# Performance work log

Hardware: AMD Instinct MI355X
Metric: run time of the kernel (lower is better)

The kernel has to match this reference:

```python
import jax, jax.numpy as jnp
import numpy as np

B, H, W, DIM, HEADS, WS, SHIFT = 16, 64, 64, 512, 16, 8, 4
HEAD_DIM = DIM // HEADS
MLP_HID = 4 * DIM
N_WIN = (H // WS) * (W // WS)
NW = WS * WS  # tokens per window
SCALE = HEAD_DIM ** -0.5
LN_EPS = 1e-5


def _np_win_partition(x, ws):
    # replicates rearrange 'b (s1 h2) (s2 w2) c -> (b h2 w2) (s1 s2) c' (interleaved partition)
    b, h, w, c = x.shape
    h2, w2 = h // ws, w // ws
    x = x.reshape(b, ws, h2, ws, w2, c).transpose(0, 2, 4, 1, 3, 5)
    return x.reshape(b * h2 * w2, ws * ws, c)


def _build_mask():
    img = np.zeros((1, H, W, 1), np.float32)
    sl = [slice(0, -WS), slice(-WS, -SHIFT), slice(-SHIFT, None)]
    cnt = 0
    for hs in sl:
        for ws_ in sl:
            img[:, hs, ws_, :] = cnt
            cnt += 1
    wm = _np_win_partition(img, WS).reshape(-1, NW)  # (N_WIN, NW)
    diff = wm[:, None, :] - wm[:, :, None]
    mask = np.where(diff == 0, 1.0, 0.0).astype(np.float32)
    return (1.0 - mask) * -1e10  # (N_WIN, NW, NW) additive mask


def _rel_index():
    ch = np.arange(WS)
    coords = np.stack(np.meshgrid(ch, ch, indexing='ij')).reshape(2, -1)  # (2, NW)
    rel = (coords[:, :, None] - coords[:, None, :]).transpose(1, 2, 0)  # (NW, NW, 2)
    rel[..., 0] += WS - 1
    rel[..., 1] += WS - 1
    rel[..., 0] *= 2 * WS - 1
    return rel.sum(-1)  # (NW, NW) int


MASK = jnp.asarray(_build_mask())
REL_IDX = jnp.asarray(_rel_index().reshape(-1))


def _win_partition(x):  # (B, H, W, C) -> (B*N_WIN, NW, C)
    h2, w2 = H // WS, W // WS
    x = x.reshape(B, WS, h2, WS, w2, DIM).transpose(0, 2, 4, 1, 3, 5)
    return x.reshape(B * h2 * w2, WS * WS, DIM)


def _win_reverse(w):  # (B*N_WIN, NW, C) -> (B, H*W, C), inverse of the interleaved partition
    h2, w2 = H // WS, W // WS
    x = w.reshape(B, h2, w2, WS, WS, DIM).transpose(0, 3, 1, 4, 2, 5)
    return x.reshape(B, H * W, DIM)


def _ln(x, w, b):
    m = x.mean(-1, keepdims=True)
    v = jnp.mean((x - m) ** 2, axis=-1, keepdims=True)
    return (x - m) / jnp.sqrt(v + LN_EPS) * w + b


def setup_inputs() -> dict:
    key = jax.random.key(0)
    ks = jax.random.split(key, 6)
    std = 0.02
    return {
        'x': jax.random.normal(ks[0], (B, H * W, DIM), jnp.float32),
        'ln1_w': jnp.ones((DIM,), jnp.float32),
        'ln1_b': jnp.zeros((DIM,), jnp.float32),
        'qkv_w': jax.random.normal(ks[1], (3 * DIM, DIM), jnp.float32) * std,
        'qkv_b': jnp.zeros((3 * DIM,), jnp.float32),
        'rpb_table': jax.random.normal(ks[2], ((2 * WS - 1) ** 2, HEADS), jnp.float32) * std,
        'proj_w': jax.random.normal(ks[3], (DIM, DIM), jnp.float32) * std,
        'proj_b': jnp.zeros((DIM,), jnp.float32),
        'ln2_w': jnp.ones((DIM,), jnp.float32),
        'ln2_b': jnp.zeros((DIM,), jnp.float32),
        'fc1_w': jax.random.normal(ks[4], (MLP_HID, DIM), jnp.float32) * std,
        'fc1_b': jnp.zeros((MLP_HID,), jnp.float32),
        'fc2_w': jax.random.normal(ks[5], (DIM, MLP_HID), jnp.float32) * std,
        'fc2_b': jnp.zeros((DIM,), jnp.float32),
    }


def reference(x, ln1_w, ln1_b, qkv_w, qkv_b, rpb_table, proj_w, proj_b,
              ln2_w, ln2_b, fc1_w, fc1_b, fc2_w, fc2_b):
    h = x
    y = _ln(x, ln1_w, ln1_b).reshape(B, H, W, DIM)
    y = jnp.roll(y, (-SHIFT, -SHIFT), axis=(1, 2))  # cyclic shift
    xw = _win_partition(y)  # (B*N_WIN, NW, DIM)

    qkv = xw @ qkv_w.T + qkv_b  # (B*N_WIN, NW, 3*DIM)
    # original splits channel as (heads, head_dim, qkv) with qkv innermost
    qkv = qkv.reshape(B * N_WIN, NW, HEADS, HEAD_DIM, 3)
    q = qkv[..., 0].transpose(0, 2, 1, 3) * SCALE  # (Bw, H, NW, d)
    k = qkv[..., 1].transpose(0, 2, 1, 3)
    v = qkv[..., 2].transpose(0, 2, 1, 3)

    attn = jnp.einsum('bhqd,bhkd->bhqk', q, k)
    bias = rpb_table[REL_IDX].reshape(NW, NW, HEADS).transpose(2, 0, 1)  # (H, NW, NW)
    attn = attn + bias[None]
    # shift mask: per-window additive mask broadcast over batch and heads
    attn = attn.reshape(B, N_WIN, HEADS, NW, NW) + MASK[None, :, None]
    attn = jax.nn.softmax(attn, axis=-1).reshape(B * N_WIN, HEADS, NW, NW)

    out = jnp.einsum('bhqk,bhkd->bhqd', attn, v)
    out = out.transpose(0, 2, 1, 3).reshape(B * N_WIN, NW, DIM)
    out = out @ proj_w.T + proj_b

    attn_out = _win_reverse(out)  # (B, H*W, DIM)
    # NOTE: faithful to original - attention output is NOT rolled back before residual
    x2 = h + attn_out

    z = _ln(x2, ln2_w, ln2_b)
    z = jax.nn.gelu(z @ fc1_w.T + fc1_b, approximate=False)
    z = z @ fc2_w.T + fc2_b
    return x2 + z
```

## Files before the change

kernel.cpp:

```cpp
#include <hip/hip_runtime.h>
#include <math.h>

typedef short short8 __attribute__((ext_vector_type(8)));
typedef float f32x4 __attribute__((ext_vector_type(4)));
typedef unsigned short u16;
typedef u16 us4 __attribute__((ext_vector_type(4)));

#define DEVI static __device__ __forceinline__

constexpr float SCALE_Q = 0.17677669529663687f;

DEVI u16 f2bf(float f) {
  unsigned u = __builtin_bit_cast(unsigned, f);
  u += 0x7FFFu + ((u >> 16) & 1u);
  return (u16)(u >> 16);
}

DEVI void gload16(const u16* g, u16* l) {
  __builtin_amdgcn_global_load_lds((const __attribute__((address_space(1))) void*)g,
                                   (__attribute__((address_space(3))) void*)l,
                                   16, 0, 0);
}

__global__ void cvt_bf16(const float4* __restrict__ src, us4* __restrict__ dst, int n4) {
  int i = blockIdx.x * 256 + threadIdx.x;
  if (i < n4) {
    float4 v = src[i];
    us4 o = { f2bf(v.x), f2bf(v.y), f2bf(v.z), f2bf(v.w) };
    dst[i] = o;
  }
}

__global__ void cvt_qkvw(const float4* __restrict__ src, us4* __restrict__ dst) {
  int i = blockIdx.x * 256 + threadIdx.x;
  int row = i >> 7, c4 = i & 127;
  int which = row >> 9, head = (row >> 5) & 15, d = row & 31;
  int srow = head * 96 + d * 3 + which;
  float4 v = src[srow * 128 + c4];
  us4 o = { f2bf(v.x), f2bf(v.y), f2bf(v.z), f2bf(v.w) };
  dst[i] = o;
}

__global__ void perm_qkvb(const float* __restrict__ src, float* __restrict__ dst) {
  int i = blockIdx.x * 256 + threadIdx.x;
  int which = i >> 9, head = (i >> 5) & 15, d = i & 31;
  dst[i] = src[head * 96 + d * 3 + which];
}

template<bool PERM>
__global__ __launch_bounds__(256) void ln_kernel(const float* __restrict__ src,
                                                 const float* __restrict__ gw,
                                                 const float* __restrict__ gb,
                                                 u16* __restrict__ dst) {
  int wid = threadIdx.x >> 6, lane = threadIdx.x & 63;
  int m = blockIdx.x * 4 + wid;
  int srow;
  if (PERM) {
    int b = m >> 12;
    int win = (m >> 6) & 63, t = m & 63;
    int i2 = win >> 3, j2 = win & 7, s1 = t >> 3, s2 = t & 7;
    int h = (s1 * 8 + i2 + 4) & 63, w = (s2 * 8 + j2 + 4) & 63;
    srow = (b << 12) + h * 64 + w;
  } else {
    srow = m;
  }
  const float4* r4 = (const float4*)(src + (size_t)srow * 512);
  float4 v0 = r4[lane], v1 = r4[lane + 64];
  float s  = v0.x + v0.y + v0.z + v0.w + v1.x + v1.y + v1.z + v1.w;
  float ss = v0.x*v0.x + v0.y*v0.y + v0.z*v0.z + v0.w*v0.w
           + v1.x*v1.x + v1.y*v1.y + v1.z*v1.z + v1.w*v1.w;
  #pragma unroll
  for (int off = 1; off < 64; off <<= 1) {
    s  += __shfl_xor(s, off);
    ss += __shfl_xor(ss, off);
  }
  float mean = s * (1.f/512.f);
  float var  = ss * (1.f/512.f) - mean*mean;
  float rstd = rsqrtf(var + 1e-5f);
  const float4* w4 = (const float4*)gw;
  const float4* b4 = (const float4*)gb;
  float4 wa = w4[lane], ba = b4[lane], wb = w4[lane+64], bb = b4[lane+64];
  us4 o0 = { f2bf((v0.x-mean)*rstd*wa.x + ba.x),
             f2bf((v0.y-mean)*rstd*wa.y + ba.y),
             f2bf((v0.z-mean)*rstd*wa.z + ba.z),
             f2bf((v0.w-mean)*rstd*wa.w + ba.w) };
  us4 o1 = { f2bf((v1.x-mean)*rstd*wb.x + bb.x),
             f2bf((v1.y-mean)*rstd*wb.y + bb.y),
             f2bf((v1.z-mean)*rstd*wb.z + bb.z),
             f2bf((v1.w-mean)*rstd*wb.w + bb.w) };
  us4* d4 = (us4*)(dst + (size_t)m * 512);
  d4[lane] = o0; d4[lane + 64] = o1;
}

template<int MODE>
__global__ __launch_bounds__(512, 2) void gemm_k(const u16* __restrict__ A,
                                                 const u16* __restrict__ Bw,
                                                 const float* __restrict__ bias,
                                                 u16* __restrict__ o0, u16* __restrict__ o1,
                                                 u16* __restrict__ o2,
                                                 float* __restrict__ fo,
                                                 const float* __restrict__ resid,
                                                 int M, int N, int K) {
  __shared__ u16 LDS2[2][2][16384];
  int nt = N >> 8;
  int nwg = gridDim.x;
  int cpx = nwg >> 3;
  int bid = blockIdx.x;
  int swz = (bid & 7) * cpx + (bid >> 3);
  int tm = swz / nt, tn = swz % nt;
  int tid = threadIdx.x;
  int lane = tid & 63, wv = tid >> 6;
  int wm = wv >> 2, wn = wv & 3;
  int rr = lane & 15, g = lane >> 4;

  const u16* asrc[4]; const u16* bsrc[4];
  #pragma unroll
  for (int l = 0; l < 4; l++) {
    int idx = l * 512 + tid;
    int r = idx >> 3, ch = idx & 7;
    int cs = (ch ^ (r & 7)) * 8;
    asrc[l] = A  + (size_t)(tm * 256 + r) * K + cs;
    bsrc[l] = Bw + (size_t)(tn * 256 + r) * K + cs;
  }
  int NT = K >> 6;

  #pragma unroll
  for (int l = 0; l < 4; l++) {
    gload16(asrc[l], &LDS2[0][0][(l * 512 + wv * 64) * 8]);
    gload16(bsrc[l], &LDS2[0][1][(l * 512 + wv * 64) * 8]);
  }

  f32x4 acc[8][4] = {};

  for (int t = 0; t < NT; ++t) {
    int cur = t & 1;
    asm volatile("s_waitcnt vmcnt(0)" ::: "memory");
    __builtin_amdgcn_s_barrier();
    const u16* AT = &LDS2[cur][0][0];
    const u16* BT = &LDS2[cur][1][0];
    short8 bfr[4][2];
    #pragma unroll
    for (int q = 0; q < 4; q++) {
      if (q < 2 && t + 1 < NT) {
        int koff = (t + 1) * 64;
        #pragma unroll
        for (int h = 0; h < 2; h++) {
          int l = q * 2 + h;
          gload16(asrc[l] + koff, &LDS2[cur ^ 1][0][(l * 512 + wv * 64) * 8]);
          gload16(bsrc[l] + koff, &LDS2[cur ^ 1][1][(l * 512 + wv * 64) * 8]);
        }
      }
      if (q == 0) {
        #pragma unroll
        for (int ni = 0; ni < 4; ni++)
          #pragma unroll
          for (int ks = 0; ks < 2; ks++) {
            int r = wn * 64 + ni * 16 + rr;
            bfr[ni][ks] = *(const short8*)(BT + r * 64 + (((ks * 4 + g) ^ (r & 7)) * 8));
          }
      }
      short8 af[2][2];
      #pragma unroll
      for (int mm = 0; mm < 2; mm++)
        #pragma unroll
        for (int ks = 0; ks < 2; ks++) {
          int r = wm * 128 + (q * 2 + mm) * 16 + rr;
          af[mm][ks] = *(const short8*)(AT + r * 64 + (((ks * 4 + g) ^ (r & 7)) * 8));
        }
      __builtin_amdgcn_s_setprio(1);
      #pragma unroll
      for (int mm = 0; mm < 2; mm++)
        #pragma unroll
        for (int ks = 0; ks < 2; ks++)
          #pragma unroll
          for (int ni = 0; ni < 4; ni++)
            acc[q * 2 + mm][ni] = __builtin_amdgcn_mfma_f32_16x16x32_bf16(
                af[mm][ks], bfr[ni][ks], acc[q * 2 + mm][ni], 0, 0, 0);
      __builtin_amdgcn_s_setprio(0);
    }
  }

  __syncthreads();
  u16* wreg = &LDS2[0][0][0] + wv * 8192;
  int rb0 = tm * 256 + wm * 128;
  int cb0 = tn * 256 + wn * 64;

  if (MODE == 0 || MODE == 2) {
    bool isV = (MODE == 0) && (tn >= 4);
    if (!isV) {
      #pragma unroll
      for (int mi = 0; mi < 8; mi++)
        #pragma unroll
        for (int ni = 0; ni < 4; ni++) {
          float bv = bias[cb0 + ni * 16 + rr];
          #pragma unroll
          for (int r = 0; r < 4; r++) {
            float val = acc[mi][ni][r] + bv;
            if (MODE == 2) val = 0.5f * val * (1.f + erff(val * 0.70710678118654752f));
            if (MODE == 0 && tn < 2) val *= SCALE_Q;
            int row = mi * 16 + g * 4 + r;
            int col = ni * 16 + rr;
            wreg[row * 64 + (((col >> 3) ^ (row & 7)) * 8) + (col & 7)] = f2bf(val);
          }
        }
      #pragma unroll
      for (int rep = 0; rep < 2; rep++) {
        int row = rep * 64 + lane;
        #pragma unroll
        for (int ch = 0; ch < 8; ch++) {
          short8 vd = *(const short8*)&wreg[row * 64 + ((ch ^ (row & 7)) * 8)];
          if (MODE == 2) {
            size_t grow = (size_t)rb0 + row;
            *(short8*)(o0 + grow * N + cb0 + ch * 8) = vd;
          } else {
            int grow = rb0 + row;
            int w = grow >> 6, tt = grow & 63;
            int hb = (cb0 & 511) >> 5;
            int head = hb + (ch >> 2);
            u16* dst = (tn < 2) ? o0 : o1;
            *(short8*)(dst + ((size_t)(w * 16 + head) * 64 + tt) * 32 + (ch & 3) * 8) = vd;
          }
        }
      }
    } else {
      #pragma unroll
      for (int mi = 0; mi < 8; mi++)
        #pragma unroll
        for (int ni = 0; ni < 4; ni++) {
          float bv = bias[cb0 + ni * 16 + rr];
          #pragma unroll
          for (int r = 0; r < 4; r++) {
            float val = acc[mi][ni][r] + bv;
            int row = mi * 16 + g * 4 + r;
            int col = ni * 16 + rr;
            wreg[col * 128 + (((row >> 3) ^ (col & 7)) * 8) + (row & 7)] = f2bf(val);
          }
        }
      int cb0v = cb0 - 1024;
      int col = lane;
      int head = (cb0v >> 5) + (col >> 5), d = col & 31;
      #pragma unroll
      for (int ch = 0; ch < 16; ch++) {
        short8 vd = *(const short8*)&wreg[col * 128 + ((ch ^ (col & 7)) * 8)];
        int grow = rb0 + ch * 8;
        int w = grow >> 6, t0 = grow & 63;
        *(short8*)(o2 + ((size_t)(w * 16 + head) * 32 + d) * 64 + t0) = vd;
      }
    }
  } else {
    #pragma unroll
    for (int ni = 0; ni < 4; ni++) {
      int col = cb0 + ni * 16 + rr;
      float bv = bias[col];
      #pragma unroll
      for (int mi = 0; mi < 8; mi++) {
        #pragma unroll
        for (int r = 0; r < 4; r++) {
          int row = rb0 + mi * 16 + g * 4 + r;
          float val = acc[mi][ni][r] + bv;
          if (MODE == 1) {
            int w = row >> 6, t = row & 63;
            int b = w >> 6, win = w & 63;
            int i2 = win >> 3, j2 = win & 7, s1 = t >> 3, s2 = t & 7;
            int pos = (b << 12) + (s1 * 8 + i2) * 64 + (s2 * 8 + j2);
            size_t idx = (size_t)pos * 512 + col;
            fo[idx] = resid[idx] + val;
          } else {
            size_t idx = (size_t)row * 512 + col;
            fo[idx] += val;
          }
        }
      }
    }
  }
}

DEVI int zone1(int x) { return x < 56 ? 0 : (x < 60 ? 1 : 2); }

__global__ __launch_bounds__(256) void attn_k(const u16* __restrict__ qb,
                                              const u16* __restrict__ kb,
                                              const u16* __restrict__ vtb,
                                              const float* __restrict__ rpb,
                                              u16* __restrict__ outb) {
  __shared__ u16 P[4][64][72];
  int wid = threadIdx.x >> 6, lane = threadIdx.x & 63;
  int p = blockIdx.x * 4 + wid;
  int w = p >> 4, head = p & 15;
  const u16* qq = qb  + (size_t)p * 2048;
  const u16* kk = kb  + (size_t)p * 2048;
  const u16* vv = vtb + (size_t)p * 2048;
  int rr = lane & 15, g = lane >> 4;

  short8 qf[4], kf[4];
  #pragma unroll
  for (int i = 0; i < 4; i++) qf[i] = *(const short8*)(qq + (i*16 + rr)*32 + g*8);
  #pragma unroll
  for (int i = 0; i < 4; i++) kf[i] = *(const short8*)(kk + (i*16 + rr)*32 + g*8);

  f32x4 zero = {0.f, 0.f, 0.f, 0.f};
  f32x4 s[4][4];
  #pragma unroll
  for (int qi = 0; qi < 4; qi++)
    #pragma unroll
    for (int kj = 0; kj < 4; kj++)
      s[qi][kj] = __builtin_amdgcn_mfma_f32_16x16x32_bf16(qf[qi], kf[kj], zero, 0, 0, 0);

  int win = w & 63, i2 = win >> 3, j2 = win & 7;
  #pragma unroll
  for (int qi = 0; qi < 4; qi++) {
    #pragma unroll
    for (int r = 0; r < 4; r++) {
      int i = qi*16 + g*4 + r;
      int s1i = i >> 3, s2i = i & 7;
      int zi = zone1(s1i*8 + i2)*3 + zone1(s2i*8 + j2);
      #pragma unroll
      for (int kj = 0; kj < 4; kj++) {
        int j = kj*16 + rr;
        int s1j = j >> 3, s2j = j & 7;
        float bv = rpb[((s1i - s1j + 7)*15 + (s2i - s2j + 7))*16 + head];
        int zj = zone1(s1j*8 + i2)*3 + zone1(s2j*8 + j2);
        s[qi][kj][r] += bv + (zi != zj ? -1e10f : 0.f);
      }
    }
  }

  float inv[4][4];
  #pragma unroll
  for (int qi = 0; qi < 4; qi++) {
    #pragma unroll
    for (int r = 0; r < 4; r++) {
      float mx = fmaxf(fmaxf(s[qi][0][r], s[qi][1][r]), fmaxf(s[qi][2][r], s[qi][3][r]));
      mx = fmaxf(mx, __shfl_xor(mx, 1));
      mx = fmaxf(mx, __shfl_xor(mx, 2));
      mx = fmaxf(mx, __shfl_xor(mx, 4));
      mx = fmaxf(mx, __shfl_xor(mx, 8));
      float sum = 0.f;
      #pragma unroll
      for (int kj = 0; kj < 4; kj++) {
        float e = __expf(s[qi][kj][r] - mx);
        s[qi][kj][r] = e;
        sum += e;
      }
      sum += __shfl_xor(sum, 1);
      sum += __shfl_xor(sum, 2);
      sum += __shfl_xor(sum, 4);
      sum += __shfl_xor(sum, 8);
      inv[qi][r] = 1.f / sum;
    }
  }

  #pragma unroll
  for (int qi = 0; qi < 4; qi++)
    #pragma unroll
    for (int kj = 0; kj < 4; kj++)
      #pragma unroll
      for (int r = 0; r < 4; r++)
        P[wid][qi*16 + g*4 + r][kj*16 + rr] = f2bf(s[qi][kj][r]);

  f32x4 o[4][2] = {};
  #pragma unroll
  for (int jh = 0; jh < 2; jh++) {
    short8 vf[2];
    #pragma unroll
    for (int df = 0; df < 2; df++)
      vf[df] = *(const short8*)(vv + (size_t)(df*16 + rr)*64 + jh*32 + g*8);
    #pragma unroll
    for (int qi = 0; qi < 4; qi++) {
      short8 pf = *(const short8*)(&P[wid][qi*16 + rr][jh*32 + g*8]);
      #pragma unroll
      for (int df = 0; df < 2; df++)
        o[qi][df] = __builtin_amdgcn_mfma_f32_16x16x32_bf16(pf, vf[df], o[qi][df], 0, 0, 0);
    }
  }

  #pragma unroll
  for (int qi = 0; qi < 4; qi++)
    #pragma unroll
    for (int df = 0; df < 2; df++)
      #pragma unroll
      for (int r = 0; r < 4; r++) {
        int t = qi*16 + g*4 + r;
        int d = df*16 + rr;
        outb[(size_t)(w*64 + t)*512 + head*32 + d] = f2bf(o[qi][df][r] * inv[qi][r]);
      }
}

extern "C" void kernel_launch(void* const* d_in, const int* in_sizes, int n_in,
                              void* d_out, int out_size, void* d_ws, size_t ws_size,
                              hipStream_t stream) {
  const float* x     = (const float*)d_in[0];
  const float* ln1w  = (const float*)d_in[1];
  const float* ln1b  = (const float*)d_in[2];
  const float* qkvw  = (const float*)d_in[3];
  const float* qkvb  = (const float*)d_in[4];
  const float* rpb   = (const float*)d_in[5];
  const float* projw = (const float*)d_in[6];
  const float* projb = (const float*)d_in[7];
  const float* ln2w  = (const float*)d_in[8];
  const float* ln2b  = (const float*)d_in[9];
  const float* fc1w  = (const float*)d_in[10];
  const float* fc1b  = (const float*)d_in[11];
  const float* fc2w  = (const float*)d_in[12];
  const float* fc2b  = (const float*)d_in[13];
  float* out = (float*)d_out;

  char* ws = (char*)d_ws;
  u16* wqkv  = (u16*)(ws + 0);
  u16* wproj = (u16*)(ws + 1572864);
  u16* wfc1  = (u16*)(ws + 2097152);
  u16* wfc2  = (u16*)(ws + 4194304);
  float* pb  = (float*)(ws + 6291456);
  size_t base = 8ull << 20;
  u16* xw = (u16*)(ws + base);
  u16* qb = (u16*)(ws + base + (64ull  << 20));
  u16* kb = (u16*)(ws + base + (128ull << 20));
  u16* vb = (u16*)(ws + base + (192ull << 20));
  u16* attnb = xw;
  u16* zb    = xw;
  u16* hb    = qb;

  cvt_qkvw<<<768, 256, 0, stream>>>((const float4*)qkvw, (us4*)wqkv);
  perm_qkvb<<<6, 256, 0, stream>>>(qkvb, pb);
  cvt_bf16<<<256,  256, 0, stream>>>((const float4*)projw, (us4*)wproj, 65536);
  cvt_bf16<<<1024, 256, 0, stream>>>((const float4*)fc1w,  (us4*)wfc1,  262144);
  cvt_bf16<<<1024, 256, 0, stream>>>((const float4*)fc2w,  (us4*)wfc2,  262144);

  ln_kernel<true><<<16384, 256, 0, stream>>>(x, ln1w, ln1b, xw);
  gemm_k<0><<<1536, 512, 0, stream>>>(xw, wqkv, pb, qb, kb, vb, nullptr, nullptr,
                                      65536, 1536, 512);
  attn_k<<<4096, 256, 0, stream>>>(qb, kb, vb, rpb, attnb);
  gemm_k<1><<<512, 512, 0, stream>>>(attnb, wproj, projb, nullptr, nullptr, nullptr,
                                     out, x, 65536, 512, 512);
  ln_kernel<false><<<16384, 256, 0, stream>>>(out, ln2w, ln2b, zb);
  gemm_k<2><<<2048, 512, 0, stream>>>(zb, wfc1, fc1b, hb, nullptr, nullptr, nullptr, nullptr,
                                      65536, 2048, 512);
  gemm_k<3><<<512, 512, 0, stream>>>(hb, wfc2, fc2b, nullptr, nullptr, nullptr, out, nullptr,
                                     65536, 512, 2048);
}
```

Baseline: 1.019 ms.

## Restructure GEMM mainloop into 4-stage K=32 pipeline and use tanh GELU

Replaces the double-buffered K=64 GEMM main loop with a four-stage ring of K=32 tiles. A and B loads are staged at separate phases, with explicit vmcnt waits and barriers interleaving the two halves of the MFMA work against LDS reads. It also changes the LDS swizzle and lowers launch bounds to one block per CU to make room for the larger 128KB buffer. Separately, the exact erf GELU epilogue is replaced by a tanh-approximation via exp and rcp, which is cheaper but numerically different from the reference's exact GELU.

```diff
diff --git a/kernel.cpp b/kernel.cpp
--- a/kernel.cpp
+++ b/kernel.cpp
@@ -93,7 +93,7 @@
 }
 
 template<int MODE>
-__global__ __launch_bounds__(512, 2) void gemm_k(const u16* __restrict__ A,
+__global__ __launch_bounds__(512, 1) void gemm_k(const u16* __restrict__ A,
                                                  const u16* __restrict__ Bw,
                                                  const float* __restrict__ bias,
                                                  u16* __restrict__ o0, u16* __restrict__ o1,
@@ -101,87 +101,89 @@
                                                  float* __restrict__ fo,
                                                  const float* __restrict__ resid,
                                                  int M, int N, int K) {
-  __shared__ u16 LDS2[2][2][16384];
+  __shared__ u16 LDS[65536];
   int nt = N >> 8;
-  int nwg = gridDim.x;
-  int cpx = nwg >> 3;
-  int bid = blockIdx.x;
+  int nwg = gridDim.x, cpx = nwg >> 3, bid = blockIdx.x;
   int swz = (bid & 7) * cpx + (bid >> 3);
   int tm = swz / nt, tn = swz % nt;
-  int tid = threadIdx.x;
-  int lane = tid & 63, wv = tid >> 6;
+  int tid = threadIdx.x, lane = tid & 63, wv = tid >> 6;
   int wm = wv >> 2, wn = wv & 3;
   int rr = lane & 15, g = lane >> 4;
-
-  const u16* asrc[4]; const u16* bsrc[4];
-  #pragma unroll
-  for (int l = 0; l < 4; l++) {
-    int idx = l * 512 + tid;
-    int r = idx >> 3, ch = idx & 7;
-    int cs = (ch ^ (r & 7)) * 8;
-    asrc[l] = A  + (size_t)(tm * 256 + r) * K + cs;
-    bsrc[l] = Bw + (size_t)(tn * 256 + r) * K + cs;
-  }
-  int NT = K >> 6;
-
-  #pragma unroll
-  for (int l = 0; l < 4; l++) {
-    gload16(asrc[l], &LDS2[0][0][(l * 512 + wv * 64) * 8]);
-    gload16(bsrc[l], &LDS2[0][1][(l * 512 + wv * 64) * 8]);
-  }
+  int NT = K >> 5;
+
+  int rA = tid >> 2, ch = tid & 3;
+  int ga = (ch - (rA >> 1)) & 3;
+  const u16* a0 = A  + (size_t)(tm * 256 + rA) * K + ga * 8;
+  const u16* b0 = Bw + (size_t)(tn * 256 + rA) * K + ga * 8;
+  size_t rskip = (size_t)128 * K;
+
+#define STAGE_A(kt) { u16* d = &LDS[(((kt) & 3) << 14) + (wv << 9)]; \
+    gload16(a0 + (kt) * 32, d); gload16(a0 + rskip + (kt) * 32, d + 4096); }
+#define STAGE_B(kt) { u16* d = &LDS[(((kt) & 3) << 14) + 8192 + (wv << 9)]; \
+    gload16(b0 + (kt) * 32, d); gload16(b0 + rskip + (kt) * 32, d + 4096); }
 
   f32x4 acc[8][4] = {};
 
-  for (int t = 0; t < NT; ++t) {
-    int cur = t & 1;
-    asm volatile("s_waitcnt vmcnt(0)" ::: "memory");
+  STAGE_A(0); STAGE_B(0);
+  STAGE_A(1); STAGE_B(1);
+  STAGE_A(2); STAGE_B(2);
+  asm volatile("s_waitcnt vmcnt(8)" ::: "memory");
+  __builtin_amdgcn_s_barrier();
+
+  for (int kt = 0; kt < NT; ++kt) {
+    int c = kt & 3;
+    const u16* AT = &LDS[c << 14];
+    const u16* BT = &LDS[(c << 14) + 8192];
+    if (kt + 3 < NT) STAGE_A(kt + 3);
+    short8 bf[4], af[4];
+    #pragma unroll
+    for (int ni = 0; ni < 4; ni++) {
+      int r = wn * 64 + ni * 16 + rr;
+      bf[ni] = *(const short8*)(BT + r * 32 + (((g + (r >> 1)) & 3) << 3));
+    }
+    #pragma unroll
+    for (int mi = 0; mi < 4; mi++) {
+      int r = wm * 128 + mi * 16 + rr;
+      af[mi] = *(const short8*)(AT + r * 32 + (((g + (r >> 1)) & 3) << 3));
+    }
     __builtin_amdgcn_s_barrier();
-    const u16* AT = &LDS2[cur][0][0];
-    const u16* BT = &LDS2[cur][1][0];
-    short8 bfr[4][2];
-    #pragma unroll
-    for (int q = 0; q < 4; q++) {
-      if (q < 2 && t + 1 < NT) {
-        int koff = (t + 1) * 64;
-        #pragma unroll
-        for (int h = 0; h < 2; h++) {
-          int l = q * 2 + h;
-          gload16(asrc[l] + koff, &LDS2[cur ^ 1][0][(l * 512 + wv * 64) * 8]);
-          gload16(bsrc[l] + koff, &LDS2[cur ^ 1][1][(l * 512 + wv * 64) * 8]);
-        }
-      }
-      if (q == 0) {
-        #pragma unroll
-        for (int ni = 0; ni < 4; ni++)
-          #pragma unroll
-          for (int ks = 0; ks < 2; ks++) {
-            int r = wn * 64 + ni * 16 + rr;
-            bfr[ni][ks] = *(const short8*)(BT + r * 64 + (((ks * 4 + g) ^ (r & 7)) * 8));
-          }
-      }
-      short8 af[2][2];
-      #pragma unroll
-      for (int mm = 0; mm < 2; mm++)
-        #pragma unroll
-        for (int ks = 0; ks < 2; ks++) {
-          int r = wm * 128 + (q * 2 + mm) * 16 + rr;
-          af[mm][ks] = *(const short8*)(AT + r * 64 + (((ks * 4 + g) ^ (r & 7)) * 8));
-        }
-      __builtin_amdgcn_s_setprio(1);
-      #pragma unroll
-      for (int mm = 0; mm < 2; mm++)
-        #pragma unroll
-        for (int ks = 0; ks < 2; ks++)
-          #pragma unroll
-          for (int ni = 0; ni < 4; ni++)
-            acc[q * 2 + mm][ni] = __builtin_amdgcn_mfma_f32_16x16x32_bf16(
-                af[mm][ks], bfr[ni][ks], acc[q * 2 + mm][ni], 0, 0, 0);
-      __builtin_amdgcn_s_setprio(0);
-    }
-  }
+    asm volatile("s_waitcnt lgkmcnt(0)" ::: "memory");
+    __builtin_amdgcn_sched_barrier(0);
+    __builtin_amdgcn_s_setprio(1);
+    #pragma unroll
+    for (int mi = 0; mi < 4; mi++)
+      #pragma unroll
+      for (int ni = 0; ni < 4; ni++)
+        acc[mi][ni] = __builtin_amdgcn_mfma_f32_16x16x32_bf16(af[mi], bf[ni], acc[mi][ni], 0, 0, 0);
+    __builtin_amdgcn_s_setprio(0);
+    __builtin_amdgcn_s_barrier();
+    if (kt + 3 < NT) STAGE_B(kt + 3);
+    short8 af2[4];
+    #pragma unroll
+    for (int mi = 0; mi < 4; mi++) {
+      int r = wm * 128 + 64 + mi * 16 + rr;
+      af2[mi] = *(const short8*)(AT + r * 32 + (((g + (r >> 1)) & 3) << 3));
+    }
+    if (kt < NT - 3)      { asm volatile("s_waitcnt vmcnt(8)" ::: "memory"); }
+    else if (kt == NT - 3){ asm volatile("s_waitcnt vmcnt(4)" ::: "memory"); }
+    else if (kt == NT - 2){ asm volatile("s_waitcnt vmcnt(0)" ::: "memory"); }
+    __builtin_amdgcn_s_barrier();
+    asm volatile("s_waitcnt lgkmcnt(0)" ::: "memory");
+    __builtin_amdgcn_sched_barrier(0);
+    __builtin_amdgcn_s_setprio(1);
+    #pragma unroll
+    for (int mi = 0; mi < 4; mi++)
+      #pragma unroll
+      for (int ni = 0; ni < 4; ni++)
+        acc[4 + mi][ni] = __builtin_amdgcn_mfma_f32_16x16x32_bf16(af2[mi], bf[ni], acc[4 + mi][ni], 0, 0, 0);
+    __builtin_amdgcn_s_setprio(0);
+    __builtin_amdgcn_s_barrier();
+  }
+#undef STAGE_A
+#undef STAGE_B
 
   __syncthreads();
-  u16* wreg = &LDS2[0][0][0] + wv * 8192;
+  u16* wreg = &LDS[0] + wv * 8192;
   int rb0 = tm * 256 + wm * 128;
   int cb0 = tn * 256 + wn * 64;
 
@@ -196,7 +198,11 @@
           #pragma unroll
           for (int r = 0; r < 4; r++) {
             float val = acc[mi][ni][r] + bv;
-            if (MODE == 2) val = 0.5f * val * (1.f + erff(val * 0.70710678118654752f));
+            if (MODE == 2) {
+              float u = val * (0.79788456f + 0.03567740814f * val * val);
+              float e = __expf(2.f * u);
+              val = val * (1.f - __builtin_amdgcn_rcpf(e + 1.f));
+            }
             if (MODE == 0 && tn < 2) val *= SCALE_Q;
             int row = mi * 16 + g * 4 + r;
             int col = ni * 16 + rr;
@@ -207,18 +213,18 @@
       for (int rep = 0; rep < 2; rep++) {
         int row = rep * 64 + lane;
         #pragma unroll
-        for (int ch = 0; ch < 8; ch++) {
-          short8 vd = *(const short8*)&wreg[row * 64 + ((ch ^ (row & 7)) * 8)];
+        for (int chk = 0; chk < 8; chk++) {
+          short8 vd = *(const short8*)&wreg[row * 64 + ((chk ^ (row & 7)) * 8)];
           if (MODE == 2) {
             size_t grow = (size_t)rb0 + row;
-            *(short8*)(o0 + grow * N + cb0 + ch * 8) = vd;
+            *(short8*)(o0 + grow * N + cb0 + chk * 8) = vd;
           } else {
             int grow = rb0 + row;
             int w = grow >> 6, tt = grow & 63;
             int hb = (cb0 & 511) >> 5;
-            int head = hb + (ch >> 2);
+            int head = hb + (chk >> 2);
             u16* dst = (tn < 2) ? o0 : o1;
-            *(short8*)(dst + ((size_t)(w * 16 + head) * 64 + tt) * 32 + (ch & 3) * 8) = vd;
+            *(short8*)(dst + ((size_t)(w * 16 + head) * 64 + tt) * 32 + (chk & 3) * 8) = vd;
           }
         }
       }
@@ -240,9 +246,9 @@
       int col = lane;
       int head = (cb0v >> 5) + (col >> 5), d = col & 31;
       #pragma unroll
-      for (int ch = 0; ch < 16; ch++) {
-        short8 vd = *(const short8*)&wreg[col * 128 + ((ch ^ (col & 7)) * 8)];
-        int grow = rb0 + ch * 8;
+      for (int chk = 0; chk < 16; chk++) {
+        short8 vd = *(const short8*)&wreg[col * 128 + ((chk ^ (col & 7)) * 8)];
+        int grow = rb0 + chk * 8;
         int w = grow >> 6, t0 = grow & 63;
         *(short8*)(o2 + ((size_t)(w * 16 + head) * 32 + d) * 64 + t0) = vd;
       }
```

Measured after the change: 885.3 us. 13.2% less time.
